# Kernel tuning notes

Measured on AMD Instinct MI355X. Metric: run time of the kernel, lower is better.

The kernel has to match this reference:

```python
import jax, jax.numpy as jnp
import numpy as np

N = 50000
E = 800000
IN_CH = 256
HID = 32
HEADS = 4
OUT_CH = 40
NEG_SLOPE = 0.2
BN_EPS = 1e-5


def _gat_conv(x, W, att_src, att_dst, bias, src, dst, num_nodes, concat):
    # x: [N, F_in]; W: [F_in, H*C]; att_src/att_dst: [H, C]
    H, C = att_src.shape
    h = (x @ W).reshape(num_nodes, H, C)            # [N, H, C]
    a_src = (h * att_src[None]).sum(-1)             # [N, H]
    a_dst = (h * att_dst[None]).sum(-1)             # [N, H]
    e = jax.nn.leaky_relu(a_src[src] + a_dst[dst], NEG_SLOPE)  # [Etot, H]
    # segment softmax over incoming edges of each destination node
    m = jax.ops.segment_max(e, dst, num_segments=num_nodes)    # [N, H]
    ex = jnp.exp(e - m[dst])
    s = jax.ops.segment_sum(ex, dst, num_segments=num_nodes)   # [N, H]
    alpha = ex / (s[dst] + 1e-16)                   # [Etot, H]
    out = jax.ops.segment_sum(h[src] * alpha[:, :, None], dst,
                              num_segments=num_nodes)          # [N, H, C]
    out = out.reshape(num_nodes, H * C) if concat else out.mean(axis=1)
    return out + bias


def setup_inputs() -> dict:
    key = jax.random.key(0)
    ks = jax.random.split(key, 12)
    x = jax.random.normal(ks[0], (N, IN_CH), dtype=jnp.float32)
    edge_index = jax.random.randint(ks[1], (2, E), 0, N, dtype=jnp.int64)
    # layer 1: in -> heads*hid, concat
    W1 = jax.random.normal(ks[2], (IN_CH, HEADS * HID), dtype=jnp.float32) * (1.0 / np.sqrt(IN_CH))
    att_src1 = jax.random.normal(ks[3], (HEADS, HID), dtype=jnp.float32) * 0.1
    att_dst1 = jax.random.normal(ks[4], (HEADS, HID), dtype=jnp.float32) * 0.1
    b1 = jnp.zeros((HEADS * HID,), dtype=jnp.float32)
    # batch norm over hidden*heads features
    gamma = jnp.ones((HEADS * HID,), dtype=jnp.float32)
    beta = jnp.zeros((HEADS * HID,), dtype=jnp.float32)
    # layer 2: heads*hid -> out, heads=1, mean (concat=False)
    W2 = jax.random.normal(ks[5], (HEADS * HID, OUT_CH), dtype=jnp.float32) * (1.0 / np.sqrt(HEADS * HID))
    att_src2 = jax.random.normal(ks[6], (1, OUT_CH), dtype=jnp.float32) * 0.1
    att_dst2 = jax.random.normal(ks[7], (1, OUT_CH), dtype=jnp.float32) * 0.1
    b2 = jnp.zeros((OUT_CH,), dtype=jnp.float32)
    return {"x": x, "edge_index": edge_index, "W1": W1, "att_src1": att_src1,
            "att_dst1": att_dst1, "b1": b1, "gamma": gamma, "beta": beta,
            "W2": W2, "att_src2": att_src2, "att_dst2": att_dst2, "b2": b2}


def reference(x, edge_index, W1, att_src1, att_dst1, b1, gamma, beta,
              W2, att_src2, att_dst2, b2):
    num_nodes = x.shape[0]
    loops = jnp.arange(num_nodes, dtype=edge_index.dtype)
    src = jnp.concatenate([edge_index[0], loops])   # add self-loops (PyG default)
    dst = jnp.concatenate([edge_index[1], loops])
    h = _gat_conv(x, W1, att_src1, att_dst1, b1, src, dst, num_nodes, concat=True)
    # BatchNorm over nodes (training-mode batch statistics)
    mu = h.mean(axis=0)
    var = h.var(axis=0)
    h = (h - mu) * jax.lax.rsqrt(var + BN_EPS) * gamma + beta
    h = jax.nn.elu(h)
    out = _gat_conv(h, W2, att_src2, att_dst2, b2, src, dst, num_nodes, concat=False)
    return out
```

## Files before the change

### kernel.cpp

```cpp
#include <hip/hip_runtime.h>

#define NN 50000
#define EE 800000
#define FIN 256
#define F1 128
#define F2 40
#define CAP 48
#define G1B ((NN + 63) / 64)
#define FILLB ((EE + 255) / 256)
#define G1PB 3126
#define G2P0 3125
#define G2P1 ((NN + 63) / 64)
#define LSTR 56

typedef unsigned int u32;
typedef unsigned short u16;
typedef _Float16 h8 __attribute__((ext_vector_type(8)));
typedef float f4 __attribute__((ext_vector_type(4)));

static __device__ __forceinline__ u32 f2bf(float f) {
  u32 u = __float_as_uint(f);
  return (u + 0x7FFFu + ((u >> 16) & 1u)) >> 16;
}
#define BF_LO(u) __uint_as_float((u) << 16)
#define BF_HI(u) __uint_as_float((u) & 0xFFFF0000u)

static __device__ __forceinline__ int sel4i(int a, int b, int c, int d, int k) {
  int lo = (k & 1) ? b : a;
  int hi = (k & 1) ? d : c;
  return (k & 2) ? hi : lo;
}

__global__ __launch_bounds__(256) void g1f_kernel(const float* __restrict__ x,
                                                  const float* __restrict__ W1,
                                                  const float* __restrict__ att_src,
                                                  const float* __restrict__ att_dst,
                                                  u32* __restrict__ h1bf,
                                                  float* __restrict__ a_src,
                                                  float* __restrict__ a_dst,
                                                  const int* __restrict__ ei,
                                                  int* __restrict__ cnt,
                                                  u16* __restrict__ csr) {
  __shared__ __align__(16) _Float16 Alds[64 * LSTR];
  __shared__ __align__(16) _Float16 Blds[128 * LSTR];
  const int t = threadIdx.x;

  if (blockIdx.x >= G1B) {
    int e = (blockIdx.x - G1B) * 256 + t;
    if (e < EE) {
      int src = ei[e];
      int dst = ei[EE + e];
      int p = atomicAdd(cnt + dst, 1);
      if (p < CAP) csr[dst * CAP + p] = (u16)src;
    }
    return;
  }

  const int m0 = blockIdx.x * 64;
  const int l  = t & 63;
  const int w  = t >> 6;
  const int q  = l & 15;
  const int hq = l >> 4;

  const int arow  = t >> 2;
  const int akoff = (t & 3) * 8;
  const int bn    = t & 127;
  const int bkh   = (t >> 7) * 16;

  f4 acc[8] = {};

  float ax[8];
  float bx[16];
  {
    int gr = m0 + arow;
    if (gr < NN) {
      float4 u0 = *(const float4*)(x + (size_t)gr * FIN + akoff);
      float4 u1 = *(const float4*)(x + (size_t)gr * FIN + akoff + 4);
      ax[0] = u0.x; ax[1] = u0.y; ax[2] = u0.z; ax[3] = u0.w;
      ax[4] = u1.x; ax[5] = u1.y; ax[6] = u1.z; ax[7] = u1.w;
    } else {
#pragma unroll
      for (int i = 0; i < 8; ++i) ax[i] = 0.f;
    }
#pragma unroll
    for (int i = 0; i < 16; ++i) bx[i] = W1[(size_t)(bkh + i) * F1 + bn];
  }

  for (int s = 0; s < 8; ++s) {
    __syncthreads();
    {
      h8 av;
#pragma unroll
      for (int i = 0; i < 8; ++i) av[i] = (_Float16)ax[i];
      *(h8*)(Alds + arow * LSTR + akoff) = av;
      h8 bv0, bv1;
#pragma unroll
      for (int i = 0; i < 8; ++i) { bv0[i] = (_Float16)bx[i]; bv1[i] = (_Float16)bx[8 + i]; }
      *(h8*)(Blds + bn * LSTR + bkh) = bv0;
      *(h8*)(Blds + bn * LSTR + bkh + 8) = bv1;
    }
    __syncthreads();
    if (s < 7) {
      int k0 = (s + 1) * 32;
      int gr = m0 + arow;
      if (gr < NN) {
        float4 u0 = *(const float4*)(x + (size_t)gr * FIN + k0 + akoff);
        float4 u1 = *(const float4*)(x + (size_t)gr * FIN + k0 + akoff + 4);
        ax[0] = u0.x; ax[1] = u0.y; ax[2] = u0.z; ax[3] = u0.w;
        ax[4] = u1.x; ax[5] = u1.y; ax[6] = u1.z; ax[7] = u1.w;
      } else {
#pragma unroll
        for (int i = 0; i < 8; ++i) ax[i] = 0.f;
      }
#pragma unroll
      for (int i = 0; i < 16; ++i) bx[i] = W1[(size_t)(k0 + bkh + i) * F1 + bn];
    }
    h8 af = *(const h8*)(Alds + (w * 16 + q) * LSTR + hq * 8);
#pragma unroll
    for (int nf = 0; nf < 8; ++nf) {
      h8 bf = *(const h8*)(Blds + (nf * 16 + q) * LSTR + hq * 8);
      acc[nf] = __builtin_amdgcn_mfma_f32_16x16x32_f16(af, bf, acc[nf], 0, 0, 0);
    }
  }

  u16* h1u = (u16*)h1bf;
#pragma unroll
  for (int nf = 0; nf < 8; ++nf) {
    int ph = nf >> 1;
#pragma unroll
    for (int r = 0; r < 4; ++r) {
      int grow = m0 + w * 16 + hq * 4 + r;
      if (grow < NN)
        h1u[((size_t)ph * NN + grow) * 32 + (nf & 1) * 16 + q] = (u16)f2bf(acc[nf][r]);
    }
  }
  float as8[8], ad8[8];
#pragma unroll
  for (int nf = 0; nf < 8; ++nf) {
    as8[nf] = att_src[nf * 16 + q];
    ad8[nf] = att_dst[nf * 16 + q];
  }
#pragma unroll
  for (int r = 0; r < 4; ++r) {
    float p0 = acc[0][r] * as8[0] + acc[1][r] * as8[1];
    float p1 = acc[2][r] * as8[2] + acc[3][r] * as8[3];
    float p2 = acc[4][r] * as8[4] + acc[5][r] * as8[5];
    float p3 = acc[6][r] * as8[6] + acc[7][r] * as8[7];
    float d0 = acc[0][r] * ad8[0] + acc[1][r] * ad8[1];
    float d1 = acc[2][r] * ad8[2] + acc[3][r] * ad8[3];
    float d2 = acc[4][r] * ad8[4] + acc[5][r] * ad8[5];
    float d3 = acc[6][r] * ad8[6] + acc[7][r] * ad8[7];
#pragma unroll
    for (int off = 1; off < 16; off <<= 1) {
      p0 += __shfl_xor(p0, off); p1 += __shfl_xor(p1, off);
      p2 += __shfl_xor(p2, off); p3 += __shfl_xor(p3, off);
      d0 += __shfl_xor(d0, off); d1 += __shfl_xor(d1, off);
      d2 += __shfl_xor(d2, off); d3 += __shfl_xor(d3, off);
    }
    int grow = m0 + w * 16 + hq * 4 + r;
    if (grow < NN && q < 8) {
      float vs = (q & 2) ? ((q & 1) ? p3 : p2) : ((q & 1) ? p1 : p0);
      float vd = (q & 2) ? ((q & 1) ? d3 : d2) : ((q & 1) ? d1 : d0);
      if (q < 4) a_src[(size_t)q * NN + grow] = vs;
      else       a_dst[grow * 4 + (q - 4)] = vd;
    }
  }
}

__global__ __launch_bounds__(256) void gather1_kernel(const int* __restrict__ cnt,
                                                      const u16* __restrict__ csr,
                                                      const float* __restrict__ a_src,
                                                      const float* __restrict__ a_dst,
                                                      const u32* __restrict__ h1bf,
                                                      const float* __restrict__ b1,
                                                      float* __restrict__ h1b,
                                                      float* __restrict__ bnsum,
                                                      float* __restrict__ bnsq) {
  __shared__ float bns[32], bnq[32];
  __shared__ __align__(16) u16 idx[16 * CAP];
  int t = threadIdx.x;
  if (t < 32) { bns[t] = 0.f; bnq[t] = 0.f; }
  int d = blockIdx.x;
  int xcd = d & 7;
  int p = xcd >> 1;
  int nb = ((d >> 3) << 1) + (xcd & 1);
  int base_n = nb * 16;
  bool blk_ok = (nb < 3125);
  if (blk_ok && t < 96)
    ((uint4*)idx)[t] = ((const uint4*)(csr + (size_t)base_n * CAP))[t];
  __syncthreads();
  int n = base_n + (t >> 4);
  int sub = t & 15;
  int g = sub >> 2;
  int l = sub & 3;
  int f0 = p * 32 + l * 8;
  float acc[8] = {0.f, 0.f, 0.f, 0.f, 0.f, 0.f, 0.f, 0.f};
  float ssum = 0.f;
  if (blk_ok) {
    const float* asp = a_src + (size_t)p * NN;
    float adst = a_dst[n * 4 + p];
    const u32* hb = h1bf + (size_t)p * NN * 16 + l * 4;
    if (g == 0) {
      float e0 = asp[n] + adst;
      e0 = e0 > 0.f ? e0 : 0.2f * e0;
      float x0 = __expf(e0);
      uint4 qv = *(const uint4*)(hb + (size_t)n * 16);
      acc[0] = fmaf(x0, BF_LO(qv.x), acc[0]); acc[1] = fmaf(x0, BF_HI(qv.x), acc[1]);
      acc[2] = fmaf(x0, BF_LO(qv.y), acc[2]); acc[3] = fmaf(x0, BF_HI(qv.y), acc[3]);
      acc[4] = fmaf(x0, BF_LO(qv.z), acc[4]); acc[5] = fmaf(x0, BF_HI(qv.z), acc[5]);
      acc[6] = fmaf(x0, BF_LO(qv.w), acc[6]); acc[7] = fmaf(x0, BF_HI(qv.w), acc[7]);
      ssum += x0;
    }
    const u16* lrow = idx + (t >> 4) * CAP;
    int m = cnt[n]; if (m > CAP) m = CAP;
    int sp = (m + 3) >> 2;
    int i = g * sp;
    int end = i + sp; if (end > m) end = m;
    int gb = (t & 63) & ~3;
    for (; i + 3 < end; i += 4) {
      int s0 = lrow[i + 0];
      int s1 = lrow[i + 1];
      int s2 = lrow[i + 2];
      int s3 = lrow[i + 3];
      float av = asp[sel4i(s0, s1, s2, s3, l)];
      uint4 q0 = *(const uint4*)(hb + (size_t)s0 * 16);
      uint4 q1 = *(const uint4*)(hb + (size_t)s1 * 16);
      uint4 q2 = *(const uint4*)(hb + (size_t)s2 * 16);
      uint4 q3 = *(const uint4*)(hb + (size_t)s3 * 16);
      float e0 = __shfl(av, gb + 0, 64) + adst;
      float e1 = __shfl(av, gb + 1, 64) + adst;
      float e2 = __shfl(av, gb + 2, 64) + adst;
      float e3 = __shfl(av, gb + 3, 64) + adst;
      e0 = e0 > 0.f ? e0 : 0.2f * e0;  float x0 = __expf(e0);
      e1 = e1 > 0.f ? e1 : 0.2f * e1;  float x1 = __expf(e1);
      e2 = e2 > 0.f ? e2 : 0.2f * e2;  float x2 = __expf(e2);
      e3 = e3 > 0.f ? e3 : 0.2f * e3;  float x3 = __expf(e3);
      acc[0] = fmaf(x0, BF_LO(q0.x), acc[0]); acc[1] = fmaf(x0, BF_HI(q0.x), acc[1]);
      acc[2] = fmaf(x0, BF_LO(q0.y), acc[2]); acc[3] = fmaf(x0, BF_HI(q0.y), acc[3]);
      acc[4] = fmaf(x0, BF_LO(q0.z), acc[4]); acc[5] = fmaf(x0, BF_HI(q0.z), acc[5]);
      acc[6] = fmaf(x0, BF_LO(q0.w), acc[6]); acc[7] = fmaf(x0, BF_HI(q0.w), acc[7]);
      acc[0] = fmaf(x1, BF_LO(q1.x), acc[0]); acc[1] = fmaf(x1, BF_HI(q1.x), acc[1]);
      acc[2] = fmaf(x1, BF_LO(q1.y), acc[2]); acc[3] = fmaf(x1, BF_HI(q1.y), acc[3]);
      acc[4] = fmaf(x1, BF_LO(q1.z), acc[4]); acc[5] = fmaf(x1, BF_HI(q1.z), acc[5]);
      acc[6] = fmaf(x1, BF_LO(q1.w), acc[6]); acc[7] = fmaf(x1, BF_HI(q1.w), acc[7]);
      acc[0] = fmaf(x2, BF_LO(q2.x), acc[0]); acc[1] = fmaf(x2, BF_HI(q2.x), acc[1]);
      acc[2] = fmaf(x2, BF_LO(q2.y), acc[2]); acc[3] = fmaf(x2, BF_HI(q2.y), acc[3]);
      acc[4] = fmaf(x2, BF_LO(q2.z), acc[4]); acc[5] = fmaf(x2, BF_HI(q2.z), acc[5]);
      acc[6] = fmaf(x2, BF_LO(q2.w), acc[6]); acc[7] = fmaf(x2, BF_HI(q2.w), acc[7]);
      acc[0] = fmaf(x3, BF_LO(q3.x), acc[0]); acc[1] = fmaf(x3, BF_HI(q3.x), acc[1]);
      acc[2] = fmaf(x3, BF_LO(q3.y), acc[2]); acc[3] = fmaf(x3, BF_HI(q3.y), acc[3]);
      acc[4] = fmaf(x3, BF_LO(q3.z), acc[4]); acc[5] = fmaf(x3, BF_HI(q3.z), acc[5]);
      acc[6] = fmaf(x3, BF_LO(q3.w), acc[6]); acc[7] = fmaf(x3, BF_HI(q3.w), acc[7]);
      ssum += x0 + x1 + x2 + x3;
    }
    for (; i < end; ++i) {
      int s0 = lrow[i];
      float e0 = asp[s0] + adst;
      e0 = e0 > 0.f ? e0 : 0.2f * e0;
      float x0 = __expf(e0);
      uint4 qv = *(const uint4*)(hb + (size_t)s0 * 16);
      acc[0] = fmaf(x0, BF_LO(qv.x), acc[0]); acc[1] = fmaf(x0, BF_HI(qv.x), acc[1]);
      acc[2] = fmaf(x0, BF_LO(qv.y), acc[2]); acc[3] = fmaf(x0, BF_HI(qv.y), acc[3]);
      acc[4] = fmaf(x0, BF_LO(qv.z), acc[4]); acc[5] = fmaf(x0, BF_HI(qv.z), acc[5]);
      acc[6] = fmaf(x0, BF_LO(qv.w), acc[6]); acc[7] = fmaf(x0, BF_HI(qv.w), acc[7]);
      ssum += x0;
    }
  }
#pragma unroll
  for (int j = 0; j < 8; ++j) {
    acc[j] += __shfl_xor(acc[j], 4);
    acc[j] += __shfl_xor(acc[j], 8);
  }
  ssum += __shfl_xor(ssum, 4);
  ssum += __shfl_xor(ssum, 8);
  if (blk_ok && g == 0) {
    float inv = 1.f / (ssum + 1e-16f);
    float4 b0 = *(const float4*)(b1 + f0);
    float4 b4 = *(const float4*)(b1 + f0 + 4);
    float o[8];
    o[0] = acc[0] * inv + b0.x; o[1] = acc[1] * inv + b0.y;
    o[2] = acc[2] * inv + b0.z; o[3] = acc[3] * inv + b0.w;
    o[4] = acc[4] * inv + b4.x; o[5] = acc[5] * inv + b4.y;
    o[6] = acc[6] * inv + b4.z; o[7] = acc[7] * inv + b4.w;
    float4 w0 = {o[0], o[1], o[2], o[3]};
    float4 w1 = {o[4], o[5], o[6], o[7]};
    *(float4*)(h1b + (size_t)n * F1 + f0) = w0;
    *(float4*)(h1b + (size_t)n * F1 + f0 + 4) = w1;
    int lb = l * 8;
#pragma unroll
    for (int j = 0; j < 8; ++j) {
      atomicAdd(&bns[lb + j], o[j]);
      atomicAdd(&bnq[lb + j], o[j] * o[j]);
    }
  }
  __syncthreads();
  if (t < 32) {
    atomicAdd(bnsum + p * 32 + t, bns[t]);
    atomicAdd(bnsq + p * 32 + t, bnq[t]);
  }
}

__global__ __launch_bounds__(256) void gemm2_kernel(const float* __restrict__ hpre,
                                                    const float* __restrict__ W2,
                                                    const float* __restrict__ bnsum,
                                                    const float* __restrict__ bnsq,
                                                    const float* __restrict__ gamma,
                                                    const float* __restrict__ beta,
                                                    u16* __restrict__ h2a,
                                                    u16* __restrict__ h2b,
                                                    const float* __restrict__ att_src2,
                                                    const float* __restrict__ att_dst2,
                                                    float* __restrict__ a_src2,
                                                    float* __restrict__ a_dst2) {
  __shared__ float Wlds[128 * 40];
  __shared__ float Alds[16 * 128];
  __shared__ float sc[128], sh[128];
  int t = threadIdx.x;
  for (int i = t; i < 128 * 40; i += 256) Wlds[i] = W2[i];
  if (t < 128) {
    const float invN = 1.f / (float)NN;
    float mu = bnsum[t] * invN;
    float var = bnsq[t] * invN - mu * mu;
    float s = gamma[t] * rsqrtf(var + 1e-5f);
    sc[t] = s;
    sh[t] = beta[t] - mu * s;
  }
  int tr = t >> 3;
  int tc = t & 7;
  float as5[5], ad5[5];
#pragma unroll
  for (int j = 0; j < 5; ++j) { as5[j] = att_src2[tc * 5 + j]; ad5[j] = att_dst2[tc * 5 + j]; }
  int n0 = blockIdx.x * 128;
  int lrow = t >> 1;
  int lkk = (t & 1) * 8;
  float acc[4][5];
#pragma unroll
  for (int i = 0; i < 4; ++i)
#pragma unroll
    for (int j = 0; j < 5; ++j) acc[i][j] = 0.f;

  for (int k0 = 0; k0 < F1; k0 += 16) {
    float av[8];
    int gn = n0 + lrow;
    if (gn < NN) {
      float4 v0 = *(const float4*)(hpre + (size_t)gn * F1 + k0 + lkk);
      float4 v1 = *(const float4*)(hpre + (size_t)gn * F1 + k0 + lkk + 4);
      av[0] = v0.x; av[1] = v0.y; av[2] = v0.z; av[3] = v0.w;
      av[4] = v1.x; av[5] = v1.y; av[6] = v1.z; av[7] = v1.w;
    } else {
#pragma unroll
      for (int j = 0; j < 8; ++j) av[j] = 0.f;
    }
    __syncthreads();
#pragma unroll
    for (int j = 0; j < 8; ++j) {
      int kg = k0 + lkk + j;
      float a = av[j] * sc[kg] + sh[kg];
      a = a > 0.f ? a : (__expf(a) - 1.f);
      Alds[(lkk + j) * 128 + lrow] = a;
    }
    __syncthreads();
#pragma unroll
    for (int k = 0; k < 16; ++k) {
      float4 a4 = *(const float4*)(Alds + k * 128 + tr * 4);
      float aa[4] = {a4.x, a4.y, a4.z, a4.w};
      float w[5];
#pragma unroll
      for (int j = 0; j < 5; ++j) w[j] = Wlds[(k0 + k) * 40 + tc * 5 + j];
#pragma unroll
      for (int i = 0; i < 4; ++i)
#pragma unroll
        for (int j = 0; j < 5; ++j) acc[i][j] = fmaf(aa[i], w[j], acc[i][j]);
    }
  }
#pragma unroll
  for (int i = 0; i < 4; ++i) {
    int gn = n0 + tr * 4 + i;
    if (gn < NN) {
#pragma unroll
      for (int j = 0; j < 5; ++j) {
        int f = tc * 5 + j;
        u16 v = (u16)f2bf(acc[i][j]);
        if (f < 32) h2a[(size_t)gn * 32 + f] = v;
        else        h2b[(size_t)gn * 8 + (f - 32)] = v;
      }
    }
  }
#pragma unroll
  for (int i = 0; i < 4; ++i) {
    float ps = 0.f, pd = 0.f;
#pragma unroll
    for (int j = 0; j < 5; ++j) { ps += acc[i][j] * as5[j]; pd += acc[i][j] * ad5[j]; }
#pragma unroll
    for (int off = 1; off < 8; off <<= 1) {
      ps += __shfl_xor(ps, off);
      pd += __shfl_xor(pd, off);
    }
    if (tc == 0) {
      int gn = n0 + tr * 4 + i;
      if (gn < NN) { a_src2[gn] = ps; a_dst2[gn] = pd; }
    }
  }
}

__global__ __launch_bounds__(256) void gather2_kernel(const int* __restrict__ cnt,
                                                      const u16* __restrict__ csr,
                                                      const float* __restrict__ a_src,
                                                      const float* __restrict__ a_dst,
                                                      const u32* __restrict__ h2a,
                                                      const u32* __restrict__ h2b,
                                                      const float* __restrict__ b2,
                                                      float* __restrict__ out) {
  int t = threadIdx.x;
  int d = blockIdx.x;
  if (d < G2P0) {
    __shared__ __align__(16) u16 idx[16 * CAP];
    int base_n = d * 16;
    if (t < 96)
      ((uint4*)idx)[t] = ((const uint4*)(csr + (size_t)base_n * CAP))[t];
    __syncthreads();
    int n = base_n + (t >> 4);
    int sub = t & 15;
    int g = sub >> 2;
    int l = sub & 3;
    float adst = a_dst[n];
    const u32* hb = h2a + l * 4;
    float acc[8] = {0.f, 0.f, 0.f, 0.f, 0.f, 0.f, 0.f, 0.f};
    float ssum = 0.f;
    if (g == 0) {
      float e0 = a_src[n] + adst;
      e0 = e0 > 0.f ? e0 : 0.2f * e0;
      float x0 = __expf(e0);
      uint4 qv = *(const uint4*)(hb + (size_t)n * 16);
      acc[0] = fmaf(x0, BF_LO(qv.x), acc[0]); acc[1] = fmaf(x0, BF_HI(qv.x), acc[1]);
      acc[2] = fmaf(x0, BF_LO(qv.y), acc[2]); acc[3] = fmaf(x0, BF_HI(qv.y), acc[3]);
      acc[4] = fmaf(x0, BF_LO(qv.z), acc[4]); acc[5] = fmaf(x0, BF_HI(qv.z), acc[5]);
      acc[6] = fmaf(x0, BF_LO(qv.w), acc[6]); acc[7] = fmaf(x0, BF_HI(qv.w), acc[7]);
      ssum += x0;
    }
    const u16* lrow = idx + (t >> 4) * CAP;
    int m = cnt[n]; if (m > CAP) m = CAP;
    int sp = (m + 3) >> 2;
    int i = g * sp;
    int end = i + sp; if (end > m) end = m;
    int gb = (t & 63) & ~3;
    for (; i + 3 < end; i += 4) {
      int s0 = lrow[i + 0];
      int s1 = lrow[i + 1];
      int s2 = lrow[i + 2];
      int s3 = lrow[i + 3];
      float av = a_src[sel4i(s0, s1, s2, s3, l)];
      uint4 q0 = *(const uint4*)(hb + (size_t)s0 * 16);
      uint4 q1 = *(const uint4*)(hb + (size_t)s1 * 16);
      uint4 q2 = *(const uint4*)(hb + (size_t)s2 * 16);
      uint4 q3 = *(const uint4*)(hb + (size_t)s3 * 16);
      float e0 = __shfl(av, gb + 0, 64) + adst;
      float e1 = __shfl(av, gb + 1, 64) + adst;
      float e2 = __shfl(av, gb + 2, 64) + adst;
      float e3 = __shfl(av, gb + 3, 64) + adst;
      e0 = e0 > 0.f ? e0 : 0.2f * e0;  float x0 = __expf(e0);
      e1 = e1 > 0.f ? e1 : 0.2f * e1;  float x1 = __expf(e1);
      e2 = e2 > 0.f ? e2 : 0.2f * e2;  float x2 = __expf(e2);
      e3 = e3 > 0.f ? e3 : 0.2f * e3;  float x3 = __expf(e3);
      acc[0] = fmaf(x0, BF_LO(q0.x), acc[0]); acc[1] = fmaf(x0, BF_HI(q0.x), acc[1]);
      acc[2] = fmaf(x0, BF_LO(q0.y), acc[2]); acc[3] = fmaf(x0, BF_HI(q0.y), acc[3]);
      acc[4] = fmaf(x0, BF_LO(q0.z), acc[4]); acc[5] = fmaf(x0, BF_HI(q0.z), acc[5]);
      acc[6] = fmaf(x0, BF_LO(q0.w), acc[6]); acc[7] = fmaf(x0, BF_HI(q0.w), acc[7]);
      acc[0] = fmaf(x1, BF_LO(q1.x), acc[0]); acc[1] = fmaf(x1, BF_HI(q1.x), acc[1]);
      acc[2] = fmaf(x1, BF_LO(q1.y), acc[2]); acc[3] = fmaf(x1, BF_HI(q1.y), acc[3]);
      acc[4] = fmaf(x1, BF_LO(q1.z), acc[4]); acc[5] = fmaf(x1, BF_HI(q1.z), acc[5]);
      acc[6] = fmaf(x1, BF_LO(q1.w), acc[6]); acc[7] = fmaf(x1, BF_HI(q1.w), acc[7]);
      acc[0] = fmaf(x2, BF_LO(q2.x), acc[0]); acc[1] = fmaf(x2, BF_HI(q2.x), acc[1]);
      acc[2] = fmaf(x2, BF_LO(q2.y), acc[2]); acc[3] = fmaf(x2, BF_HI(q2.y), acc[3]);
      acc[4] = fmaf(x2, BF_LO(q2.z), acc[4]); acc[5] = fmaf(x2, BF_HI(q2.z), acc[5]);
      acc[6] = fmaf(x2, BF_LO(q2.w), acc[6]); acc[7] = fmaf(x2, BF_HI(q2.w), acc[7]);
      acc[0] = fmaf(x3, BF_LO(q3.x), acc[0]); acc[1] = fmaf(x3, BF_HI(q3.x), acc[1]);
      acc[2] = fmaf(x3, BF_LO(q3.y), acc[2]); acc[3] = fmaf(x3, BF_HI(q3.y), acc[3]);
      acc[4] = fmaf(x3, BF_LO(q3.z), acc[4]); acc[5] = fmaf(x3, BF_HI(q3.z), acc[5]);
      acc[6] = fmaf(x3, BF_LO(q3.w), acc[6]); acc[7] = fmaf(x3, BF_HI(q3.w), acc[7]);
      ssum += x0 + x1 + x2 + x3;
    }
    for (; i < end; ++i) {
      int s0 = lrow[i];
      float e0 = a_src[s0] + adst;
      e0 = e0 > 0.f ? e0 : 0.2f * e0;
      float x0 = __expf(e0);
      uint4 qv = *(const uint4*)(hb + (size_t)s0 * 16);
      acc[0] = fmaf(x0, BF_LO(qv.x), acc[0]); acc[1] = fmaf(x0, BF_HI(qv.x), acc[1]);
      acc[2] = fmaf(x0, BF_LO(qv.y), acc[2]); acc[3] = fmaf(x0, BF_HI(qv.y), acc[3]);
      acc[4] = fmaf(x0, BF_LO(qv.z), acc[4]); acc[5] = fmaf(x0, BF_HI(qv.z), acc[5]);
      acc[6] = fmaf(x0, BF_LO(qv.w), acc[6]); acc[7] = fmaf(x0, BF_HI(qv.w), acc[7]);
      ssum += x0;
    }
#pragma unroll
    for (int j = 0; j < 8; ++j) {
      acc[j] += __shfl_xor(acc[j], 4);
      acc[j] += __shfl_xor(acc[j], 8);
    }
    ssum += __shfl_xor(ssum, 4);
    ssum += __shfl_xor(ssum, 8);
    if (g == 0) {
      float inv = 1.f / (ssum + 1e-16f);
      int f0 = l * 8;
      float4 b0 = *(const float4*)(b2 + f0);
      float4 b4 = *(const float4*)(b2 + f0 + 4);
      float4 w0 = {acc[0] * inv + b0.x, acc[1] * inv + b0.y,
                   acc[2] * inv + b0.z, acc[3] * inv + b0.w};
      float4 w1 = {acc[4] * inv + b4.x, acc[5] * inv + b4.y,
                   acc[6] * inv + b4.z, acc[7] * inv + b4.w};
      *(float4*)(out + (size_t)n * F2 + f0) = w0;
      *(float4*)(out + (size_t)n * F2 + f0 + 4) = w1;
    }
  } else {
    int n = (d - G2P0) * 64 + (t >> 2);
    int g = t & 3;
    float acc[8] = {0.f, 0.f, 0.f, 0.f, 0.f, 0.f, 0.f, 0.f};
    float ssum = 0.f;
    if (n < NN) {
      float adst = a_dst[n];
      if (g == 0) {
        float e0 = a_src[n] + adst;
        e0 = e0 > 0.f ? e0 : 0.2f * e0;
        float x0 = __expf(e0);
        uint4 qv = *(const uint4*)(h2b + (size_t)n * 4);
        acc[0] = fmaf(x0, BF_LO(qv.x), acc[0]); acc[1] = fmaf(x0, BF_HI(qv.x), acc[1]);
        acc[2] = fmaf(x0, BF_LO(qv.y), acc[2]); acc[3] = fmaf(x0, BF_HI(qv.y), acc[3]);
        acc[4] = fmaf(x0, BF_LO(qv.z), acc[4]); acc[5] = fmaf(x0, BF_HI(qv.z), acc[5]);
        acc[6] = fmaf(x0, BF_LO(qv.w), acc[6]); acc[7] = fmaf(x0, BF_HI(qv.w), acc[7]);
        ssum += x0;
      }
      const u16* row = csr + (size_t)n * CAP;
      int m = cnt[n]; if (m > CAP) m = CAP;
      int i = g;
      for (; i + 4 < m; i += 8) {
        int s0 = row[i];
        int s1 = row[i + 4];
        float e0 = a_src[s0];
        float e1 = a_src[s1];
        uint4 q0 = *(const uint4*)(h2b + (size_t)s0 * 4);
        uint4 q1 = *(const uint4*)(h2b + (size_t)s1 * 4);
        e0 += adst; e0 = e0 > 0.f ? e0 : 0.2f * e0;  float x0 = __expf(e0);
        e1 += adst; e1 = e1 > 0.f ? e1 : 0.2f * e1;  float x1 = __expf(e1);
        acc[0] = fmaf(x0, BF_LO(q0.x), acc[0]); acc[1] = fmaf(x0, BF_HI(q0.x), acc[1]);
        acc[2] = fmaf(x0, BF_LO(q0.y), acc[2]); acc[3] = fmaf(x0, BF_HI(q0.y), acc[3]);
        acc[4] = fmaf(x0, BF_LO(q0.z), acc[4]); acc[5] = fmaf(x0, BF_HI(q0.z), acc[5]);
        acc[6] = fmaf(x0, BF_LO(q0.w), acc[6]); acc[7] = fmaf(x0, BF_HI(q0.w), acc[7]);
        acc[0] = fmaf(x1, BF_LO(q1.x), acc[0]); acc[1] = fmaf(x1, BF_HI(q1.x), acc[1]);
        acc[2] = fmaf(x1, BF_LO(q1.y), acc[2]); acc[3] = fmaf(x1, BF_HI(q1.y), acc[3]);
        acc[4] = fmaf(x1, BF_LO(q1.z), acc[4]); acc[5] = fmaf(x1, BF_HI(q1.z), acc[5]);
        acc[6] = fmaf(x1, BF_LO(q1.w), acc[6]); acc[7] = fmaf(x1, BF_HI(q1.w), acc[7]);
        ssum += x0 + x1;
      }
      for (; i < m; i += 4) {
        int s0 = row[i];
        float e0 = a_src[s0] + adst;
        e0 = e0 > 0.f ? e0 : 0.2f * e0;
        float x0 = __expf(e0);
        uint4 qv = *(const uint4*)(h2b + (size_t)s0 * 4);
        acc[0] = fmaf(x0, BF_LO(qv.x), acc[0]); acc[1] = fmaf(x0, BF_HI(qv.x), acc[1]);
        acc[2] = fmaf(x0, BF_LO(qv.y), acc[2]); acc[3] = fmaf(x0, BF_HI(qv.y), acc[3]);
        acc[4] = fmaf(x0, BF_LO(qv.z), acc[4]); acc[5] = fmaf(x0, BF_HI(qv.z), acc[5]);
        acc[6] = fmaf(x0, BF_LO(qv.w), acc[6]); acc[7] = fmaf(x0, BF_HI(qv.w), acc[7]);
        ssum += x0;
      }
    }
#pragma unroll
    for (int j = 0; j < 8; ++j) {
      acc[j] += __shfl_xor(acc[j], 1);
      acc[j] += __shfl_xor(acc[j], 2);
    }
    ssum += __shfl_xor(ssum, 1);
    ssum += __shfl_xor(ssum, 2);
    if (n < NN && g == 0) {
      float inv = 1.f / (ssum + 1e-16f);
      float4 b0 = *(const float4*)(b2 + 32);
      float4 b4 = *(const float4*)(b2 + 36);
      float4 w0 = {acc[0] * inv + b0.x, acc[1] * inv + b0.y,
                   acc[2] * inv + b0.z, acc[3] * inv + b0.w};
      float4 w1 = {acc[4] * inv + b4.x, acc[5] * inv + b4.y,
                   acc[6] * inv + b4.z, acc[7] * inv + b4.w};
      *(float4*)(out + (size_t)n * F2 + 32) = w0;
      *(float4*)(out + (size_t)n * F2 + 36) = w1;
    }
  }
}

extern "C" void kernel_launch(void* const* d_in, const int* in_sizes, int n_in,
                              void* d_out, int out_size, void* d_ws, size_t ws_size,
                              hipStream_t stream) {
  const float* x        = (const float*)d_in[0];
  const int*   ei       = (const int*)d_in[1];
  const float* W1       = (const float*)d_in[2];
  const float* att_src1 = (const float*)d_in[3];
  const float* att_dst1 = (const float*)d_in[4];
  const float* b1       = (const float*)d_in[5];
  const float* gamma    = (const float*)d_in[6];
  const float* beta     = (const float*)d_in[7];
  const float* W2       = (const float*)d_in[8];
  const float* att_src2 = (const float*)d_in[9];
  const float* att_dst2 = (const float*)d_in[10];
  const float* b2       = (const float*)d_in[11];
  float* out = (float*)d_out;

  int* cnt      = (int*)d_ws;
  float* bnsum  = (float*)(cnt + 50048);
  float* bnsq   = bnsum + 128;
  u16* csr      = (u16*)(bnsq + 128);
  u32* h1bf     = (u32*)(csr + (size_t)NN * CAP);
  float* h1b    = (float*)(h1bf + 3200000);
  u32* h2a      = (u32*)(h1b + 6400000);
  u32* h2b      = h2a + 800000;
  float* a_src1 = (float*)(h2b + 200000);
  float* a_dst1 = a_src1 + 200000;
  float* a_src2 = a_dst1 + 200000;
  float* a_dst2 = a_src2 + 50000;

  hipMemsetAsync(cnt, 0, (50048 + 256) * sizeof(int), stream);

  g1f_kernel<<<G1B + FILLB, 256, 0, stream>>>(x, W1, att_src1, att_dst1,
                                              h1bf, a_src1, a_dst1,
                                              ei, cnt, csr);
  gather1_kernel<<<(G1PB / 2) * 8, 256, 0, stream>>>(cnt, csr, a_src1, a_dst1,
                                                     h1bf, b1, h1b, bnsum, bnsq);
  gemm2_kernel<<<(NN + 127) / 128, 256, 0, stream>>>(h1b, W2, bnsum, bnsq,
                                                     gamma, beta,
                                                     (u16*)h2a, (u16*)h2b,
                                                     att_src2, att_dst2,
                                                     a_src2, a_dst2);
  gather2_kernel<<<G2P0 + G2P1, 256, 0, stream>>>(cnt, csr, a_src2, a_dst2,
                                                  h2a, h2b, b2, out);
}
```

Measured before the change: 294.3 us.

## Pack layer-2 source attention logit into padded feature rows for gather2

Layer 2's per-node source attention score is now stored inside the spare slots of the bf16 feature rows (h2a and h2b padded). gather2 reads it from the same 16-byte feature load and broadcasts it with a shuffle, so the separate random a_src lookup per edge goes away. The second part of gather2 is restructured to stage CSR indices in LDS and to use two lanes per node, splitting the 12 tail features. This grows h2b, and some lanes run predicated partial FMAs.

Measured after the change: 290.8 us. No clear change (-1.2%).

```diff
diff --git a/kernel.cpp b/kernel.cpp
--- a/kernel.cpp
+++ b/kernel.cpp
@@ -10,7 +10,7 @@
 #define FILLB ((EE + 255) / 256)
 #define G1PB 3126
 #define G2P0 3125
-#define G2P1 ((NN + 63) / 64)
+#define G2P1 ((NN + 31) / 32)
 #define LSTR 56
 
 typedef unsigned int u32;
@@ -310,7 +310,6 @@
                                                     u16* __restrict__ h2b,
                                                     const float* __restrict__ att_src2,
                                                     const float* __restrict__ att_dst2,
-                                                    float* __restrict__ a_src2,
                                                     float* __restrict__ a_dst2) {
   __shared__ float Wlds[128 * 40];
   __shared__ float Alds[16 * 128];
@@ -381,8 +380,8 @@
       for (int j = 0; j < 5; ++j) {
         int f = tc * 5 + j;
         u16 v = (u16)f2bf(acc[i][j]);
-        if (f < 32) h2a[(size_t)gn * 32 + f] = v;
-        else        h2b[(size_t)gn * 8 + (f - 32)] = v;
+        if (f < 28) h2a[(size_t)gn * 32 + f] = v;
+        else        h2b[(size_t)gn * 16 + (f - 28)] = v;
       }
     }
   }
@@ -398,14 +397,17 @@
     }
     if (tc == 0) {
       int gn = n0 + tr * 4 + i;
-      if (gn < NN) { a_src2[gn] = ps; a_dst2[gn] = pd; }
+      if (gn < NN) {
+        a_dst2[gn] = pd;
+        *(float*)(h2a + (size_t)gn * 32 + 28) = ps;
+        *(float*)(h2b + (size_t)gn * 16 + 12) = ps;
+      }
     }
   }
 }
 
 __global__ __launch_bounds__(256) void gather2_kernel(const int* __restrict__ cnt,
                                                       const u16* __restrict__ csr,
-                                                      const float* __restrict__ a_src,
                                                       const float* __restrict__ a_dst,
                                                       const u32* __restrict__ h2a,
                                                       const u32* __restrict__ h2b,
@@ -423,19 +425,23 @@
     int sub = t & 15;
     int g = sub >> 2;
     int l = sub & 3;
+    bool full = (l < 3);
     float adst = a_dst[n];
     const u32* hb = h2a + l * 4;
     float acc[8] = {0.f, 0.f, 0.f, 0.f, 0.f, 0.f, 0.f, 0.f};
     float ssum = 0.f;
+    int gb = (t & 63) & ~3;
     if (g == 0) {
-      float e0 = a_src[n] + adst;
+      uint4 qv = *(const uint4*)(hb + (size_t)n * 16);
+      float e0 = __shfl(__uint_as_float(qv.z), gb + 3, 64) + adst;
       e0 = e0 > 0.f ? e0 : 0.2f * e0;
       float x0 = __expf(e0);
-      uint4 qv = *(const uint4*)(hb + (size_t)n * 16);
       acc[0] = fmaf(x0, BF_LO(qv.x), acc[0]); acc[1] = fmaf(x0, BF_HI(qv.x), acc[1]);
       acc[2] = fmaf(x0, BF_LO(qv.y), acc[2]); acc[3] = fmaf(x0, BF_HI(qv.y), acc[3]);
-      acc[4] = fmaf(x0, BF_LO(qv.z), acc[4]); acc[5] = fmaf(x0, BF_HI(qv.z), acc[5]);
-      acc[6] = fmaf(x0, BF_LO(qv.w), acc[6]); acc[7] = fmaf(x0, BF_HI(qv.w), acc[7]);
+      if (full) {
+        acc[4] = fmaf(x0, BF_LO(qv.z), acc[4]); acc[5] = fmaf(x0, BF_HI(qv.z), acc[5]);
+        acc[6] = fmaf(x0, BF_LO(qv.w), acc[6]); acc[7] = fmaf(x0, BF_HI(qv.w), acc[7]);
+      }
       ssum += x0;
     }
     const u16* lrow = idx + (t >> 4) * CAP;
@@ -443,53 +449,55 @@
     int sp = (m + 3) >> 2;
     int i = g * sp;
     int end = i + sp; if (end > m) end = m;
-    int gb = (t & 63) & ~3;
     for (; i + 3 < end; i += 4) {
       int s0 = lrow[i + 0];
       int s1 = lrow[i + 1];
       int s2 = lrow[i + 2];
       int s3 = lrow[i + 3];
-      float av = a_src[sel4i(s0, s1, s2, s3, l)];
       uint4 q0 = *(const uint4*)(hb + (size_t)s0 * 16);
       uint4 q1 = *(const uint4*)(hb + (size_t)s1 * 16);
       uint4 q2 = *(const uint4*)(hb + (size_t)s2 * 16);
       uint4 q3 = *(const uint4*)(hb + (size_t)s3 * 16);
-      float e0 = __shfl(av, gb + 0, 64) + adst;
-      float e1 = __shfl(av, gb + 1, 64) + adst;
-      float e2 = __shfl(av, gb + 2, 64) + adst;
-      float e3 = __shfl(av, gb + 3, 64) + adst;
+      float e0 = __shfl(__uint_as_float(q0.z), gb + 3, 64) + adst;
+      float e1 = __shfl(__uint_as_float(q1.z), gb + 3, 64) + adst;
+      float e2 = __shfl(__uint_as_float(q2.z), gb + 3, 64) + adst;
+      float e3 = __shfl(__uint_as_float(q3.z), gb + 3, 64) + adst;
       e0 = e0 > 0.f ? e0 : 0.2f * e0;  float x0 = __expf(e0);
       e1 = e1 > 0.f ? e1 : 0.2f * e1;  float x1 = __expf(e1);
       e2 = e2 > 0.f ? e2 : 0.2f * e2;  float x2 = __expf(e2);
       e3 = e3 > 0.f ? e3 : 0.2f * e3;  float x3 = __expf(e3);
       acc[0] = fmaf(x0, BF_LO(q0.x), acc[0]); acc[1] = fmaf(x0, BF_HI(q0.x), acc[1]);
       acc[2] = fmaf(x0, BF_LO(q0.y), acc[2]); acc[3] = fmaf(x0, BF_HI(q0.y), acc[3]);
-      acc[4] = fmaf(x0, BF_LO(q0.z), acc[4]); acc[5] = fmaf(x0, BF_HI(q0.z), acc[5]);
-      acc[6] = fmaf(x0, BF_LO(q0.w), acc[6]); acc[7] = fmaf(x0, BF_HI(q0.w), acc[7]);
       acc[0] = fmaf(x1, BF_LO(q1.x), acc[0]); acc[1] = fmaf(x1, BF_HI(q1.x), acc[1]);
       acc[2] = fmaf(x1, BF_LO(q1.y), acc[2]); acc[3] = fmaf(x1, BF_HI(q1.y), acc[3]);
-      acc[4] = fmaf(x1, BF_LO(q1.z), acc[4]); acc[5] = fmaf(x1, BF_HI(q1.z), acc[5]);
-      acc[6] = fmaf(x1, BF_LO(q1.w), acc[6]); acc[7] = fmaf(x1, BF_HI(q1.w), acc[7]);
       acc[0] = fmaf(x2, BF_LO(q2.x), acc[0]); acc[1] = fmaf(x2, BF_HI(q2.x), acc[1]);
       acc[2] = fmaf(x2, BF_LO(q2.y), acc[2]); acc[3] = fmaf(x2, BF_HI(q2.y), acc[3]);
-      acc[4] = fmaf(x2, BF_LO(q2.z), acc[4]); acc[5] = fmaf(x2, BF_HI(q2.z), acc[5]);
-      acc[6] = fmaf(x2, BF_LO(q2.w), acc[6]); acc[7] = fmaf(x2, BF_HI(q2.w), acc[7]);
       acc[0] = fmaf(x3, BF_LO(q3.x), acc[0]); acc[1] = fmaf(x3, BF_HI(q3.x), acc[1]);
       acc[2] = fmaf(x3, BF_LO(q3.y), acc[2]); acc[3] = fmaf(x3, BF_HI(q3.y), acc[3]);
-      acc[4] = fmaf(x3, BF_LO(q3.z), acc[4]); acc[5] = fmaf(x3, BF_HI(q3.z), acc[5]);
-      acc[6] = fmaf(x3, BF_LO(q3.w), acc[6]); acc[7] = fmaf(x3, BF_HI(q3.w), acc[7]);
+      if (full) {
+        acc[4] = fmaf(x0, BF_LO(q0.z), acc[4]); acc[5] = fmaf(x0, BF_HI(q0.z), acc[5]);
+        acc[6] = fmaf(x0, BF_LO(q0.w), acc[6]); acc[7] = fmaf(x0, BF_HI(q0.w), acc[7]);
+        acc[4] = fmaf(x1, BF_LO(q1.z), acc[4]); acc[5] = fmaf(x1, BF_HI(q1.z), acc[5]);
+        acc[6] = fmaf(x1, BF_LO(q1.w), acc[6]); acc[7] = fmaf(x1, BF_HI(q1.w), acc[7]);
+        acc[4] = fmaf(x2, BF_LO(q2.z), acc[4]); acc[5] = fmaf(x2, BF_HI(q2.z), acc[5]);
+        acc[6] = fmaf(x2, BF_LO(q2.w), acc[6]); acc[7] = fmaf(x2, BF_HI(q2.w), acc[7]);
+        acc[4] = fmaf(x3, BF_LO(q3.z), acc[4]); acc[5] = fmaf(x3, BF_HI(q3.z), acc[5]);
+        acc[6] = fmaf(x3, BF_LO(q3.w), acc[6]); acc[7] = fmaf(x3, BF_HI(q3.w), acc[7]);
+      }
       ssum += x0 + x1 + x2 + x3;
     }
     for (; i < end; ++i) {
       int s0 = lrow[i];
-      float e0 = a_src[s0] + adst;
+      uint4 qv = *(const uint4*)(hb + (size_t)s0 * 16);
+      float e0 = __shfl(__uint_as_float(qv.z), gb + 3, 64) + adst;
       e0 = e0 > 0.f ? e0 : 0.2f * e0;
       float x0 = __expf(e0);
-      uint4 qv = *(const uint4*)(hb + (size_t)s0 * 16);
       acc[0] = fmaf(x0, BF_LO(qv.x), acc[0]); acc[1] = fmaf(x0, BF_HI(qv.x), acc[1]);
       acc[2] = fmaf(x0, BF_LO(qv.y), acc[2]); acc[3] = fmaf(x0, BF_HI(qv.y), acc[3]);
-      acc[4] = fmaf(x0, BF_LO(qv.z), acc[4]); acc[5] = fmaf(x0, BF_HI(qv.z), acc[5]);
-      acc[6] = fmaf(x0, BF_LO(qv.w), acc[6]); acc[7] = fmaf(x0, BF_HI(qv.w), acc[7]);
+      if (full) {
+        acc[4] = fmaf(x0, BF_LO(qv.z), acc[4]); acc[5] = fmaf(x0, BF_HI(qv.z), acc[5]);
+        acc[6] = fmaf(x0, BF_LO(qv.w), acc[6]); acc[7] = fmaf(x0, BF_HI(qv.w), acc[7]);
+      }
       ssum += x0;
     }
 #pragma unroll
@@ -501,86 +509,116 @@
     ssum += __shfl_xor(ssum, 8);
     if (g == 0) {
       float inv = 1.f / (ssum + 1e-16f);
-      int f0 = l * 8;
-      float4 b0 = *(const float4*)(b2 + f0);
-      float4 b4 = *(const float4*)(b2 + f0 + 4);
-      float4 w0 = {acc[0] * inv + b0.x, acc[1] * inv + b0.y,
-                   acc[2] * inv + b0.z, acc[3] * inv + b0.w};
-      float4 w1 = {acc[4] * inv + b4.x, acc[5] * inv + b4.y,
-                   acc[6] * inv + b4.z, acc[7] * inv + b4.w};
-      *(float4*)(out + (size_t)n * F2 + f0) = w0;
-      *(float4*)(out + (size_t)n * F2 + f0 + 4) = w1;
+      if (full) {
+        int f0 = l * 8;
+        float4 b0 = *(const float4*)(b2 + f0);
+        float4 b4 = *(const float4*)(b2 + f0 + 4);
+        float4 w0 = {acc[0] * inv + b0.x, acc[1] * inv + b0.y,
+                     acc[2] * inv + b0.z, acc[3] * inv + b0.w};
+        float4 w1 = {acc[4] * inv + b4.x, acc[5] * inv + b4.y,
+                     acc[6] * inv + b4.z, acc[7] * inv + b4.w};
+        *(float4*)(out + (size_t)n * F2 + f0) = w0;
+        *(float4*)(out + (size_t)n * F2 + f0 + 4) = w1;
+      } else {
+        float4 b0 = *(const float4*)(b2 + 24);
+        float4 w0 = {acc[0] * inv + b0.x, acc[1] * inv + b0.y,
+                     acc[2] * inv + b0.z, acc[3] * inv + b0.w};
+        *(float4*)(out + (size_t)n * F2 + 24) = w0;
+      }
     }
   } else {
-    int n = (d - G2P0) * 64 + (t >> 2);
-    int g = t & 3;
+    __shared__ __align__(16) u16 idx[32 * CAP];
+    int base_n = (d - G2P0) * 32;
+    if (t < 192)
+      ((uint4*)idx)[t] = ((const uint4*)(csr + (size_t)base_n * CAP))[t];
+    __syncthreads();
+    int n = base_n + (t >> 3);
+    int sub = t & 7;
+    int g = sub >> 1;
+    int l = sub & 1;
+    bool full = (l == 0);
+    int pb = (t & 63) & ~1;
     float acc[8] = {0.f, 0.f, 0.f, 0.f, 0.f, 0.f, 0.f, 0.f};
     float ssum = 0.f;
     if (n < NN) {
       float adst = a_dst[n];
+      const u32* hx = h2b + l * 4;
       if (g == 0) {
-        float e0 = a_src[n] + adst;
+        uint4 qv = *(const uint4*)(hx + (size_t)n * 8);
+        float e0 = __shfl(__uint_as_float(qv.z), pb + 1, 64) + adst;
         e0 = e0 > 0.f ? e0 : 0.2f * e0;
         float x0 = __expf(e0);
-        uint4 qv = *(const uint4*)(h2b + (size_t)n * 4);
         acc[0] = fmaf(x0, BF_LO(qv.x), acc[0]); acc[1] = fmaf(x0, BF_HI(qv.x), acc[1]);
         acc[2] = fmaf(x0, BF_LO(qv.y), acc[2]); acc[3] = fmaf(x0, BF_HI(qv.y), acc[3]);
-        acc[4] = fmaf(x0, BF_LO(qv.z), acc[4]); acc[5] = fmaf(x0, BF_HI(qv.z), acc[5]);
-        acc[6] = fmaf(x0, BF_LO(qv.w), acc[6]); acc[7] = fmaf(x0, BF_HI(qv.w), acc[7]);
+        if (full) {
+          acc[4] = fmaf(x0, BF_LO(qv.z), acc[4]); acc[5] = fmaf(x0, BF_HI(qv.z), acc[5]);
+          acc[6] = fmaf(x0, BF_LO(qv.w), acc[6]); acc[7] = fmaf(x0, BF_HI(qv.w), acc[7]);
+        }
         ssum += x0;
       }
-      const u16* row = csr + (size_t)n * CAP;
+      const u16* lrow = idx + (t >> 3) * CAP;
       int m = cnt[n]; if (m > CAP) m = CAP;
       int i = g;
       for (; i + 4 < m; i += 8) {
-        int s0 = row[i];
-        int s1 = row[i + 4];
-        float e0 = a_src[s0];
-        float e1 = a_src[s1];
-        uint4 q0 = *(const uint4*)(h2b + (size_t)s0 * 4);
-        uint4 q1 = *(const uint4*)(h2b + (size_t)s1 * 4);
-        e0 += adst; e0 = e0 > 0.f ? e0 : 0.2f * e0;  float x0 = __expf(e0);
-        e1 += adst; e1 = e1 > 0.f ? e1 : 0.2f * e1;  float x1 = __expf(e1);
+        int s0 = lrow[i];
+        int s1 = lrow[i + 4];
+        uint4 q0 = *(const uint4*)(hx + (size_t)s0 * 8);
+        uint4 q1 = *(const uint4*)(hx + (size_t)s1 * 8);
+        float e0 = __shfl(__uint_as_float(q0.z), pb + 1, 64) + adst;
+        float e1 = __shfl(__uint_as_float(q1.z), pb + 1, 64) + adst;
+        e0 = e0 > 0.f ? e0 : 0.2f * e0;  float x0 = __expf(e0);
+        e1 = e1 > 0.f ? e1 : 0.2f * e1;  float x1 = __expf(e1);
         acc[0] = fmaf(x0, BF_LO(q0.x), acc[0]); acc[1] = fmaf(x0, BF_HI(q0.x), acc[1]);
         acc[2] = fmaf(x0, BF_LO(q0.y), acc[2]); acc[3] = fmaf(x0, BF_HI(q0.y), acc[3]);
-        acc[4] = fmaf(x0, BF_LO(q0.z), acc[4]); acc[5] = fmaf(x0, BF_HI(q0.z), acc[5]);
-        acc[6] = fmaf(x0, BF_LO(q0.w), acc[6]); acc[7] = fmaf(x0, BF_HI(q0.w), acc[7]);
         acc[0] = fmaf(x1, BF_LO(q1.x), acc[0]); acc[1] = fmaf(x1, BF_HI(q1.x), acc[1]);
         acc[2] = fmaf(x1, BF_LO(q1.y), acc[2]); acc[3] = fmaf(x1, BF_HI(q1.y), acc[3]);
-        acc[4] = fmaf(x1, BF_LO(q1.z), acc[4]); acc[5] = fmaf(x1, BF_HI(q1.z), acc[5]);
-        acc[6] = fmaf(x1, BF_LO(q1.w), acc[6]); acc[7] = fmaf(x1, BF_HI(q1.w), acc[7]);
+        if (full) {
+          acc[4] = fmaf(x0, BF_LO(q0.z), acc[4]); acc[5] = fmaf(x0, BF_HI(q0.z), acc[5]);
+          acc[6] = fmaf(x0, BF_LO(q0.w), acc[6]); acc[7] = fmaf(x0, BF_HI(q0.w), acc[7]);
+          acc[4] = fmaf(x1, BF_LO(q1.z), acc[4]); acc[5] = fmaf(x1, BF_HI(q1.z), acc[5]);
+          acc[6] = fmaf(x1, BF_LO(q1.w), acc[6]); acc[7] = fmaf(x1, BF_HI(q1.w), acc[7]);
+        }
         ssum += x0 + x1;
       }
       for (; i < m; i += 4) {
-        int s0 = row[i];
-        float e0 = a_src[s0] + adst;
+        int s0 = lrow[i];
+        uint4 qv = *(const uint4*)(hx + (size_t)s0 * 8);
+        float e0 = __shfl(__uint_as_float(qv.z), pb + 1, 64) + adst;
         e0 = e0 > 0.f ? e0 : 0.2f * e0;
         float x0 = __expf(e0);
-        uint4 qv = *(const uint4*)(h2b + (size_t)s0 * 4);
         acc[0] = fmaf(x0, BF_LO(qv.x), acc[0]); acc[1] = fmaf(x0, BF_HI(qv.x), acc[1]);
         acc[2] = fmaf(x0, BF_LO(qv.y), acc[2]); acc[3] = fmaf(x0, BF_HI(qv.y), acc[3]);
-        acc[4] = fmaf(x0, BF_LO(qv.z), acc[4]); acc[5] = fmaf(x0, BF_HI(qv.z), acc[5]);
-        acc[6] = fmaf(x0, BF_LO(qv.w), acc[6]); acc[7] = fmaf(x0, BF_HI(qv.w), acc[7]);
+        if (full) {
+          acc[4] = fmaf(x0, BF_LO(qv.z), acc[4]); acc[5] = fmaf(x0, BF_HI(qv.z), acc[5]);
+          acc[6] = fmaf(x0, BF_LO(qv.w), acc[6]); acc[7] = fmaf(x0, BF_HI(qv.w), acc[7]);
+        }
         ssum += x0;
       }
     }
 #pragma unroll
     for (int j = 0; j < 8; ++j) {
-      acc[j] += __shfl_xor(acc[j], 1);
       acc[j] += __shfl_xor(acc[j], 2);
-    }
-    ssum += __shfl_xor(ssum, 1);
+      acc[j] += __shfl_xor(acc[j], 4);
+    }
     ssum += __shfl_xor(ssum, 2);
+    ssum += __shfl_xor(ssum, 4);
     if (n < NN && g == 0) {
       float inv = 1.f / (ssum + 1e-16f);
-      float4 b0 = *(const float4*)(b2 + 32);
-      float4 b4 = *(const float4*)(b2 + 36);
-      float4 w0 = {acc[0] * inv + b0.x, acc[1] * inv + b0.y,
-                   acc[2] * inv + b0.z, acc[3] * inv + b0.w};
-      float4 w1 = {acc[4] * inv + b4.x, acc[5] * inv + b4.y,
-                   acc[6] * inv + b4.z, acc[7] * inv + b4.w};
-      *(float4*)(out + (size_t)n * F2 + 32) = w0;
-      *(float4*)(out + (size_t)n * F2 + 36) = w1;
+      if (full) {
+        float4 b0 = *(const float4*)(b2 + 28);
+        float4 b4 = *(const float4*)(b2 + 32);
+        float4 w0 = {acc[0] * inv + b0.x, acc[1] * inv + b0.y,
+                     acc[2] * inv + b0.z, acc[3] * inv + b0.w};
+        float4 w1 = {acc[4] * inv + b4.x, acc[5] * inv + b4.y,
+                     acc[6] * inv + b4.z, acc[7] * inv + b4.w};
+        *(float4*)(out + (size_t)n * F2 + 28) = w0;
+        *(float4*)(out + (size_t)n * F2 + 32) = w1;
+      } else {
+        float4 b0 = *(const float4*)(b2 + 36);
+        float4 w0 = {acc[0] * inv + b0.x, acc[1] * inv + b0.y,
+                     acc[2] * inv + b0.z, acc[3] * inv + b0.w};
+        *(float4*)(out + (size_t)n * F2 + 36) = w0;
+      }
     }
   }
 }
@@ -610,10 +648,9 @@
   float* h1b    = (float*)(h1bf + 3200000);
   u32* h2a      = (u32*)(h1b + 6400000);
   u32* h2b      = h2a + 800000;
-  float* a_src1 = (float*)(h2b + 200000);
+  float* a_src1 = (float*)(h2b + 400000);
   float* a_dst1 = a_src1 + 200000;
-  float* a_src2 = a_dst1 + 200000;
-  float* a_dst2 = a_src2 + 50000;
+  float* a_dst2 = a_dst1 + 200000;
 
   hipMemsetAsync(cnt, 0, (50048 + 256) * sizeof(int), stream);
 
@@ -626,7 +663,7 @@
                                                      gamma, beta,
                                                      (u16*)h2a, (u16*)h2b,
                                                      att_src2, att_dst2,
-                                                     a_src2, a_dst2);
-  gather2_kernel<<<G2P0 + G2P1, 256, 0, stream>>>(cnt, csr, a_src2, a_dst2,
+                                                     a_dst2);
+  gather2_kernel<<<G2P0 + G2P1, 256, 0, stream>>>(cnt, csr, a_dst2,
                                                   h2a, h2b, b2, out);
 }
```
